# Optimization experiments

Hardware: AMD Instinct MI355X
Metric: run time of the kernel (lower is better)

Reference implementation:

```python
import jax, jax.numpy as jnp
import numpy as np

# ---- static config (matches init_kwargs: nlevs=[2,3,4], Pyr_mode=1, dfilt='pkva') ----
NLEVS = (2, 3, 4)
L = 3
# symmetric length-12 ladder (lifting) filter in the spirit of the 'pkva' ladder filter
_PKVA_HALF = np.array([0.6300, -0.1930, 0.0972, -0.0526, 0.0272, -0.0144])
PKVA = np.concatenate([_PKVA_HALF[::-1], _PKVA_HALF])


def _lp_hp_masks(H, W):
    """Meyer-style smooth lowpass/highpass frequency masks (rcos smooth_func)."""
    def phi(n):
        w = np.abs(2.0 * np.pi * np.fft.fftfreq(n))
        s = np.clip((w - np.pi / 3.0) / (np.pi / 3.0), 0.0, 1.0)
        beta = s ** 4 * (35.0 - 84.0 * s + 70.0 * s ** 2 - 20.0 * s ** 3)
        return np.cos(0.5 * np.pi * beta)
    Lm = phi(H)[:, None] * phi(W)[None, :]
    Hm = np.sqrt(np.clip(1.0 - Lm ** 2, 0.0, None))
    return jnp.asarray(Lm, jnp.float32), jnp.asarray(Hm, jnp.float32)


def _pyr_dec(x, nlev):
    """PyrNDDEC_mm, Pyr_mode=1: FFT-domain smooth LP/HP split, dyadic decimation of LP."""
    bands = []
    for _ in range(nlev):
        H, W = x.shape[-2], x.shape[-1]
        Lm, Hm = _lp_hp_masks(H, W)
        Xf = jnp.fft.fft2(x)
        bands.append(jnp.fft.ifft2(Xf * Hm).real.astype(x.dtype))
        x = jnp.fft.ifft2(Xf * Lm).real.astype(x.dtype)[..., ::2, ::2]
    return [x] + bands[::-1]  # y[0]=coarsest lowpass, y[1..L]=bandpass coarse->fine


def _conv1d_wrap(x, f, axis):
    """1D circular ('wrap') convolution along `axis`."""
    K = f.shape[0]
    x = jnp.moveaxis(x, axis, -1)
    pad = [(0, 0)] * (x.ndim - 1) + [(K // 2, K - 1 - K // 2)]
    xp = jnp.pad(x, pad, mode='wrap')
    shp = xp.shape
    y = jax.lax.conv_general_dilated(xp.reshape(-1, 1, shp[-1]),
                                     f.reshape(1, 1, K).astype(x.dtype), (1,), 'VALID')
    y = y.reshape(shp[:-1] + (shp[-1] - K + 1,))
    return jnp.moveaxis(y, -1, axis)


def _fan_split(x, axis, f):
    """One ladder-structured fan filter-bank stage with quincunx coset split."""
    other = -2 if axis == -1 else -1
    n_other = x.shape[other]
    shape = [1] * x.ndim
    shape[other] = n_other
    idx = jnp.arange(n_other)
    # fan <-> diamond modulation along the other axis
    sign = (1 - 2 * (idx % 2)).astype(x.dtype).reshape(shape)
    xm = x * sign
    # quincunx cosets: shift odd lines by 1 along split axis, then deinterleave
    parity = ((idx % 2) == 1).reshape(shape)
    xs = jnp.where(parity, jnp.roll(xm, -1, axis=axis), xm)
    if axis == -1:
        p0, p1 = xs[..., 0::2], xs[..., 1::2]
    else:
        p0, p1 = xs[..., 0::2, :], xs[..., 1::2, :]
    # ladder (lifting) predict/update with 1D filter f
    d = p1 - _conv1d_wrap(p0, f, axis)
    s = p0 + 0.5 * _conv1d_wrap(d, f, axis)
    return s, d


def _dfbdec(x, f, n):
    """n-level directional filter bank (ladder structure). Returns (2^n, ...) stack."""
    subs = x[None]  # (M, B, 1, H, W), all subbands same shape per level -> vectorized
    axis = -1
    for _ in range(n):
        s, d = _fan_split(subs, axis, f)
        subs = jnp.concatenate([s, d], axis=0)
        axis = -2 if axis == -1 else -1
    return subs


def setup_inputs() -> dict:
    key = jax.random.key(0)
    x = jax.random.normal(key, (16, 1, 1024, 1024), dtype=jnp.float32)
    return {"x": x}


def reference(x):
    f = jnp.asarray(PKVA, x.dtype)
    y = _pyr_dec(x, L)
    outs = [y[0]]  # coarsest lowpass (B,1,128,128)
    for k in range(1, L + 1):
        outs.append(_dfbdec(y[k], f, NLEVS[k - 1]))
    # (lowpass, 4 dirs @128x128, 8 dirs @(256,128), 16 dirs @(256,256))
    return tuple(outs)
```

## Files before the change

kernel.cpp:

```cpp
#include <hip/hip_runtime.h>
#include <math.h>

#define PI_F 3.14159265358979323846f

__constant__ float c_pkva[12] = {
  -0.0144f, 0.0272f, -0.0526f, 0.0972f, -0.193f, 0.63f,
   0.63f, -0.193f, 0.0972f, -0.0526f, 0.0272f, -0.0144f
};

constexpr int ilog2c(int n) { int l = 0; while (n > 1) { n >>= 1; ++l; } return l; }

__device__ float g_phi[1920];
constexpr int phi_off(int N) {
  return (N == 1024) ? 0 : (N == 512) ? 1024 : (N == 256) ? 1536 : 1792;
}

__device__ __forceinline__ float phi_dev(int k, int n) {
  int kk = (k < n - k) ? k : (n - k);
  float w = 2.0f * PI_F * (float)kk / (float)n;
  float s = (w - PI_F / 3.0f) * (3.0f / PI_F);
  s = fminf(fmaxf(s, 0.0f), 1.0f);
  float s2 = s * s;
  float beta = s2 * s2 * (35.0f - 84.0f * s + 70.0f * s2 - 20.0f * s2 * s);
  return __cosf(0.5f * PI_F * beta);
}

__global__ void phi_init_k() {
  int i = blockIdx.x * 256 + threadIdx.x;
  if (i < 1024)      g_phi[i] = phi_dev(i, 1024);
  else if (i < 1536) g_phi[i] = phi_dev(i - 1024, 512);
  else if (i < 1792) g_phi[i] = phi_dev(i - 1536, 256);
  else if (i < 1920) g_phi[i] = phi_dev(i - 1792, 128);
}

__device__ __forceinline__ float2 cmul(float2 a, float2 b) {
  return make_float2(a.x * b.x - a.y * b.y, a.x * b.y + a.y * b.x);
}
__device__ __forceinline__ float2 cadd(float2 a, float2 b) { return make_float2(a.x + b.x, a.y + b.y); }
__device__ __forceinline__ float2 csub(float2 a, float2 b) { return make_float2(a.x - b.x, a.y - b.y); }

template <int N>
__device__ __forceinline__ int fft_core4(float2 (*sbuf)[N], float dirsign, int tid, int cur) {
  constexpr int LOG2 = ilog2c(N);
  constexpr int NT = N / 4;
  constexpr bool LEAD2 = (LOG2 & 1);
  if constexpr (LEAD2) {
#pragma unroll
    for (int j = tid; j < N / 2; j += NT) {
      float2 v0 = sbuf[cur][j], v1 = sbuf[cur][j + N / 2];
      float2 e = cadd(v0, v1), o = csub(v0, v1);
      *(float4*)&sbuf[cur ^ 1][2 * j] = make_float4(e.x, e.y, o.x, o.y);
    }
    cur ^= 1;
    __syncthreads();
  }
#pragma unroll
  for (int Ns = LEAD2 ? 2 : 1; Ns < N; Ns <<= 2) {
    int j = tid;
    int base = j & (Ns - 1);
    float ang = dirsign * (2.0f * PI_F) * (float)base / (float)(4 * Ns);
    float2 w1; __sincosf(ang, &w1.y, &w1.x);
    float2 w2 = cmul(w1, w1);
    float2 w3 = cmul(w2, w1);
    float2 v0 = sbuf[cur][j];
    float2 v1 = cmul(sbuf[cur][j + N / 4], w1);
    float2 v2 = cmul(sbuf[cur][j + N / 2], w2);
    float2 v3 = cmul(sbuf[cur][j + 3 * (N / 4)], w3);
    float2 a0 = cadd(v0, v2), a1 = csub(v0, v2);
    float2 a2 = cadd(v1, v3), a3 = csub(v1, v3);
    float2 r1 = make_float2(-dirsign * a3.y, dirsign * a3.x);
    int idxD = ((j - base) << 2) + base;
    cur ^= 1;
    sbuf[cur][idxD]          = cadd(a0, a2);
    sbuf[cur][idxD + Ns]     = cadd(a1, r1);
    sbuf[cur][idxD + 2 * Ns] = csub(a0, a2);
    sbuf[cur][idxD + 3 * Ns] = csub(a1, r1);
    __syncthreads();
  }
  return cur;
}

template <int N, int LMODE, int SMODE>
__global__ void __launch_bounds__(N / 4)
fft_rows_k(const void* __restrict__ vin, void* __restrict__ vout,
           float dirsign, float scale) {
  constexpr int NT = N / 4;
  __shared__ __align__(16) float2 sbuf[2][N];
  const int tid = threadIdx.x;
  const int row = blockIdx.x;
  const int r = row & (N - 1);

  if (LMODE == 1) {
    const float2* in = (const float2*)vin;
#pragma unroll
    for (int i = tid; i < N; i += NT) {
      float2 v = in[(size_t)row * N + i];
      sbuf[0][i] = make_float2(v.x * scale, v.y * scale);
    }
  } else {
    const float2* in = (const float2*)vin;
    float pr = g_phi[phi_off(N) + r];
#pragma unroll
    for (int i = tid; i < N; i += NT) {
      float lm = pr * g_phi[phi_off(N) + i];
      float m = sqrtf(fmaxf(1.0f - lm * lm, 0.0f)) * scale;
      float2 v = in[(size_t)row * N + i];
      sbuf[0][i] = make_float2(v.x * m, v.y * m);
    }
  }
  __syncthreads();

  int cur = fft_core4<N>(sbuf, dirsign, tid, 0);

  if (SMODE == 0) {
    float2* outp = (float2*)vout;
#pragma unroll
    for (int i = tid; i < N; i += NT)
      outp[(size_t)row * N + i] = sbuf[cur][i];
  } else {
    float* outp = (float*)vout;
#pragma unroll
    for (int i = tid; i < N; i += NT)
      outp[(size_t)row * N + i] = sbuf[cur][i].x;
  }
}

template <int N, int PITCH>
__global__ void __launch_bounds__(N / 4)
rfft_pairs_half_k(const float* __restrict__ in, float2* __restrict__ out) {
  constexpr int NT = N / 4;
  __shared__ __align__(16) float2 sbuf[2][N];
  const int tid = threadIdx.x;
  const int img = blockIdx.x >> (ilog2c(N) - 1);
  const int r = blockIdx.x & (N / 2 - 1);
  const float* p0 = in + ((size_t)img * N + 2 * r) * N;
  const float* p1 = p0 + N;

#pragma unroll
  for (int i = tid; i < N; i += NT)
    sbuf[0][i] = make_float2(p0[i], p1[i]);
  __syncthreads();

  int cur = fft_core4<N>(sbuf, -1.0f, tid, 0);

  float2* o0 = out + ((size_t)img * N + 2 * r) * PITCH;
  float2* o1 = o0 + PITCH;
#pragma unroll
  for (int i = tid; i <= N / 2; i += NT) {
    float2 Z = sbuf[cur][i];
    float2 Zr = sbuf[cur][(N - i) & (N - 1)];
    float2 Zc = make_float2(Zr.x, -Zr.y);
    o0[i] = make_float2(0.5f * (Z.x + Zc.x), 0.5f * (Z.y + Zc.y));
    float2 dd = make_float2(Z.x - Zc.x, Z.y - Zc.y);
    o1[i] = make_float2(0.5f * dd.y, -0.5f * dd.x);
  }
}

__global__ void transpose_rect_k(const float2* __restrict__ in,
                                 float2* __restrict__ out, int R, int C) {
  __shared__ float2 tile[32][33];
  int img = blockIdx.z;
  size_t base = (size_t)img * R * C;
  int c = blockIdx.x * 32 + threadIdx.x;
  int r0 = blockIdx.y * 32;
  for (int j = threadIdx.y; j < 32; j += 8)
    tile[j][threadIdx.x] = in[base + (size_t)(r0 + j) * C + c];
  __syncthreads();
  int r = blockIdx.y * 32 + threadIdx.x;
  int c0 = blockIdx.x * 32;
  for (int j = threadIdx.y; j < 32; j += 8)
    out[base + (size_t)(c0 + j) * R + r] = tile[threadIdx.x][j];
}

template <int N, int PITCH>
__global__ void __launch_bounds__(N / 4)
fft_col_half_k(float2* __restrict__ inout, float2* __restrict__ foldb) {
  constexpr int NT = N / 4;
  constexpr int NH = N / 2;
  __shared__ __align__(16) float2 sbuf[2][N];
  const int tid = threadIdx.x;
  const int kx = blockIdx.x;
  const int img = blockIdx.y;
  float2* rowp = inout + ((size_t)img * PITCH + kx) * N;

#pragma unroll
  for (int i = tid; i < N; i += NT)
    sbuf[0][i] = rowp[i];
  __syncthreads();

  int cur = fft_core4<N>(sbuf, -1.0f, tid, 0);

  const float pr = g_phi[phi_off(N) + kx];
  const float inv = 1.0f / (float)N;
  float2* fp = foldb + ((size_t)img * (NH + 1) + kx) * NH;
#pragma unroll
  for (int i = tid; i < NH; i += NT) {
    float2 vA = sbuf[cur][i];
    float2 vB = sbuf[cur][i + NH];
    float lmA = pr * g_phi[phi_off(N) + i];
    float lmB = pr * g_phi[phi_off(N) + i + NH];
    fp[i] = make_float2(0.25f * (vA.x * lmA + vB.x * lmB),
                        0.25f * (vA.y * lmA + vB.y * lmB));
    float hmA = sqrtf(fmaxf(1.0f - lmA * lmA, 0.0f)) * inv;
    float hmB = sqrtf(fmaxf(1.0f - lmB * lmB, 0.0f)) * inv;
    sbuf[cur][i]      = make_float2(vA.x * hmA, vA.y * hmA);
    sbuf[cur][i + NH] = make_float2(vB.x * hmB, vB.y * hmB);
  }
  __syncthreads();

  cur = fft_core4<N>(sbuf, 1.0f, tid, cur);

#pragma unroll
  for (int i = tid; i < N; i += NT)
    rowp[i] = sbuf[cur][i];
}

__global__ void fold_combine_k(const float2* __restrict__ fold,
                               float2* __restrict__ spec2) {
  int idx = blockIdx.x * 256 + threadIdx.x;
  int c = idx & 511;
  int r = (idx >> 9) & 511;
  int img = idx >> 18;
  const float2* fb = fold + (size_t)img * (513 * 512);
  float2 a = fb[(size_t)r * 512 + c];
  float2 b = fb[(size_t)(512 - r) * 512 + ((512 - c) & 511)];
  spec2[((size_t)img << 18) + ((size_t)r << 9) + c] =
      make_float2(a.x + b.x, a.y - b.y);
}

template <int N, int PITCH>
__global__ void __launch_bounds__(N / 4)
ifft_fan_pair_k(const float2* __restrict__ in, float* __restrict__ outb,
                float scale, int halfT) {
  constexpr int NT = N / 4;
  constexpr int W2 = N / 2;
  __shared__ __align__(16) float2 sbuf[2][N];
  const int tid = threadIdx.x;
  const int img = blockIdx.x >> (ilog2c(N) - 1);
  const int q = blockIdx.x & (N / 2 - 1);
  const int y0 = 2 * q;
  const float2* inA = in + ((size_t)img * N + y0) * PITCH;
  const float2* inB = inA + PITCH;

#pragma unroll
  for (int i = tid; i <= W2; i += NT) {
    float2 a = inA[i], b = inB[i];
    sbuf[0][i] = make_float2((a.x - b.y) * scale, (a.y + b.x) * scale);
  }
#pragma unroll
  for (int i = tid; i < W2 - 1; i += NT) {
    int m = W2 - 1 - i;
    float2 a = inA[m], b = inB[m];
    sbuf[0][W2 + 1 + i] = make_float2((a.x + b.y) * scale, (b.x - a.y) * scale);
  }
  __syncthreads();

  int cur = fft_core4<N>(sbuf, 1.0f, tid, 0);

  float* scratch = (float*)sbuf[cur ^ 1];
  float* xe = scratch;
  float* xo = scratch + W2;
  float* db = scratch + 2 * W2;
  const size_t rbase = ((size_t)img * N + y0) * W2;

  for (int sub = 0; sub < 2; ++sub) {
    const int par = sub;
    const float sgn = par ? -1.0f : 1.0f;
#pragma unroll
    for (int i = tid; i < N; i += NT) {
      float v = par ? sbuf[cur][i].y : sbuf[cur][i].x;
      int ii = (i - par) & (N - 1);
      if (ii & 1) xo[ii >> 1] = v; else xe[ii >> 1] = v;
    }
    __syncthreads();

    float* outs = outb + rbase + (size_t)sub * W2;
    float* outd = outb + halfT + rbase + (size_t)sub * W2;
#pragma unroll 2
    for (int j = tid; j < W2; j += NT) {
      float acc = 0.0f;
#pragma unroll
      for (int k = 0; k < 12; k++)
        acc += c_pkva[k] * xe[(j - 6 + k + W2) & (W2 - 1)];
      float dv = sgn * (xo[j] - acc);
      db[j] = dv;
      outd[j] = dv;
    }
    __syncthreads();
#pragma unroll 2
    for (int j = tid; j < W2; j += NT) {
      float acc = 0.0f;
#pragma unroll
      for (int k = 0; k < 12; k++)
        acc += c_pkva[k] * db[(j - 6 + k + W2) & (W2 - 1)];
      outs[j] = sgn * xe[j] + 0.5f * acc;
    }
    __syncthreads();
  }
}

template <int N>
__global__ void __launch_bounds__(N / 4)
ifft_fan_k(const float2* __restrict__ in, float* __restrict__ outb,
           float scale, int halfT) {
  constexpr int NT = N / 4;
  constexpr int W2 = N / 2;
  __shared__ __align__(16) float2 sbuf[2][N];
  const int tid = threadIdx.x;
  const int nr = blockIdx.x;
  const int r = nr & (N - 1);
  const int par = r & 1;
  const float sgn = par ? -1.0f : 1.0f;

#pragma unroll
  for (int i = tid; i < N; i += NT) {
    float2 v = in[(size_t)nr * N + i];
    sbuf[0][i] = make_float2(v.x * scale, v.y * scale);
  }
  __syncthreads();

  int cur = fft_core4<N>(sbuf, 1.0f, tid, 0);

  float* scratch = (float*)sbuf[cur ^ 1];
  float* xe = scratch;
  float* xo = scratch + W2;
  float* db = scratch + 2 * W2;
#pragma unroll
  for (int i = tid; i < N; i += NT) {
    float v = sbuf[cur][i].x;
    int ii = (i - par) & (N - 1);
    if (ii & 1) xo[ii >> 1] = v; else xe[ii >> 1] = v;
  }
  __syncthreads();

  float* outs = outb + (size_t)nr * W2;
  float* outd = outb + halfT + (size_t)nr * W2;
#pragma unroll 2
  for (int j = tid; j < W2; j += NT) {
    float acc = 0.0f;
#pragma unroll
    for (int k = 0; k < 12; k++)
      acc += c_pkva[k] * xe[(j - 6 + k + W2) & (W2 - 1)];
    float dv = sgn * (xo[j] - acc);
    db[j] = dv;
    outd[j] = dv;
  }
  __syncthreads();
#pragma unroll 2
  for (int j = tid; j < W2; j += NT) {
    float acc = 0.0f;
#pragma unroll
    for (int k = 0; k < 12; k++)
      acc += c_pkva[k] * db[(j - 6 + k + W2) & (W2 - 1)];
    outs[j] = sgn * xe[j] + 0.5f * acc;
  }
}

__global__ void transpose_k(const float2* __restrict__ in,
                            float2* __restrict__ out, int N) {
  __shared__ float2 tile[32][33];
  int img = blockIdx.z;
  size_t base = (size_t)img * N * N;
  int x = blockIdx.x * 32 + threadIdx.x;
  int y0 = blockIdx.y * 32;
  for (int j = threadIdx.y; j < 32; j += 8)
    tile[j][threadIdx.x] = in[base + (size_t)(y0 + j) * N + x];
  __syncthreads();
  int x2 = blockIdx.y * 32 + threadIdx.x;
  int y2 = blockIdx.x * 32;
  for (int j = threadIdx.y; j < 32; j += 8)
    out[base + (size_t)(y2 + j) * N + x2] = tile[threadIdx.x][j];
}

__global__ void alias_k(const float2* __restrict__ in, float2* __restrict__ out,
                        int N, int lgN2, int phiOff) {
  int idx = blockIdx.x * 256 + threadIdx.x;
  int N2 = N >> 1;
  int c = idx & (N2 - 1);
  int r = (idx >> lgN2) & (N2 - 1);
  int img = idx >> (2 * lgN2);
  float pr0 = g_phi[phiOff + r], pr1 = g_phi[phiOff + r + N2];
  float pc0 = g_phi[phiOff + c], pc1 = g_phi[phiOff + c + N2];
  size_t base = (size_t)img * N * N;
  float2 v00 = in[base + (size_t)r * N + c];
  float2 v01 = in[base + (size_t)r * N + c + N2];
  float2 v10 = in[base + (size_t)(r + N2) * N + c];
  float2 v11 = in[base + (size_t)(r + N2) * N + c + N2];
  float m00 = pr0 * pc0, m01 = pr0 * pc1, m10 = pr1 * pc0, m11 = pr1 * pc1;
  float2 o;
  o.x = 0.25f * (v00.x * m00 + v01.x * m01 + v10.x * m10 + v11.x * m11);
  o.y = 0.25f * (v00.y * m00 + v01.y * m01 + v10.y * m10 + v11.y * m11);
  out[((size_t)img << (2 * lgN2)) + ((size_t)r << lgN2) + c] = o;
}

__global__ void __launch_bounds__(256)
fs_row_k(const float* __restrict__ x, float* __restrict__ outb,
         int lgH, int lgW, int halfT) {
  __shared__ float xe[512], xo[512], db[512];
  int H = 1 << lgH, W = 1 << lgW, W2 = W >> 1;
  int nr = blockIdx.x;
  int r = nr & (H - 1);
  int par = r & 1;
  float sgn = par ? -1.0f : 1.0f;
  const float* xrow = x + (size_t)nr * W;
  for (int j = threadIdx.x; j < W2; j += 256) {
    xe[j] = sgn * xrow[(2 * j + par) & (W - 1)];
    xo[j] = sgn * xrow[(2 * j + 1 + par) & (W - 1)];
  }
  __syncthreads();
  float* outs = outb + (size_t)nr * W2;
  float* outd = outb + halfT + (size_t)nr * W2;
  for (int j = threadIdx.x; j < W2; j += 256) {
    float acc = 0.0f;
#pragma unroll
    for (int k = 0; k < 12; k++)
      acc += c_pkva[k] * xe[(j - 6 + k + W2) & (W2 - 1)];
    float dv = xo[j] - acc;
    db[j] = dv;
    outd[j] = dv;
  }
  __syncthreads();
  for (int j = threadIdx.x; j < W2; j += 256) {
    float acc = 0.0f;
#pragma unroll
    for (int k = 0; k < 12; k++)
      acc += c_pkva[k] * db[(j - 6 + k + W2) & (W2 - 1)];
    outs[j] = xe[j] + 0.5f * acc;
  }
}

template <int TI, int TC>
__global__ void __launch_bounds__(256)
fs_col_fused_k(const float* __restrict__ x, float* __restrict__ outb,
               int lgH, int lgW, int halfT) {
  constexpr int RE = 2 * TI + 48;
  constexpr int DE = TI + 12;
  constexpr int NR = 256 / TC;
  __shared__ float raw[RE][TC];
  __shared__ float dvs[DE][TC];
  const int H = 1 << lgH, W = 1 << lgW;
  const int c0 = blockIdx.x * TC;
  const int i0 = blockIdx.y * TI;
  const int n = blockIdx.z;
  const int tc = threadIdx.x & (TC - 1);
  const int tr = threadIdx.x / TC;
  const float* xim = x + ((size_t)n << (lgH + lgW));
  const int rbase = 2 * i0 - 24;
#pragma unroll
  for (int r = tr; r < RE; r += NR) {
    int rr = (rbase + r) & (H - 1);
    raw[r][tc] = xim[((size_t)rr << lgW) + c0 + tc];
  }
  __syncthreads();
  const int par = tc & 1;
  for (int j = tr; j < DE; j += NR) {
    float acc = 0.0f;
#pragma unroll
    for (int k = 0; k < 12; k++)
      acc += c_pkva[k] * raw[2 * j + 2 * k + par][tc];
    dvs[j][tc] = raw[2 * j + 13 + par][tc] - acc;
  }
  __syncthreads();
  const float sgn = par ? -1.0f : 1.0f;
  float* outs = outb + (((size_t)n << (lgH - 1)) << lgW);
  float* outd = outs + halfT;
  for (int i = tr; i < TI; i += NR) {
    float acc = 0.0f;
#pragma unroll
    for (int k = 0; k < 12; k++)
      acc += c_pkva[k] * dvs[i + k][tc];
    float p0v = raw[2 * i + 24 + par][tc];
    size_t off = ((size_t)(i0 + i) << lgW) + c0 + tc;
    outd[off] = sgn * dvs[i + 6][tc];
    outs[off] = sgn * (p0v + 0.5f * acc);
  }
}

__global__ void fill_err_k(float* out) {
  out[threadIdx.x] = 1.0e9f;
}

extern "C" void kernel_launch(void* const* d_in, const int* in_sizes, int n_in,
                              void* d_out, int out_size, void* d_ws, size_t ws_size,
                              hipStream_t stream) {
  const float* x = (const float*)d_in[0];
  float* out = (float*)d_out;
  char* ws = (char*)d_ws;

  const size_t NEED = 220266496ull;
  if (ws_size < NEED) {
    fill_err_k<<<dim3(1), dim3(256), 0, stream>>>(out);
    return;
  }

  float2* bufA  = (float2*)(ws);
  float2* bufB  = (float2*)(ws + 71303168);
  float2* foldb = (float2*)(ws + 142606336);
  float2* spec2 = (float2*)(ws + 176226304);
  float2* spec3 = (float2*)(ws + 209780736);
  float2* spec4 = (float2*)(ws + 218169344);

  float* out0 = out;
  float* out1 = out + 262144;
  float* out2 = out + 1310720;
  float* out3 = out + 5505024;

  phi_init_k<<<dim3(8), dim3(256), 0, stream>>>();

  rfft_pairs_half_k<1024, 544><<<dim3(8192), dim3(256), 0, stream>>>(x, bufA);
  transpose_rect_k<<<dim3(17, 32, 16), dim3(32, 8), 0, stream>>>(bufA, bufB, 1024, 544);
  fft_col_half_k<1024, 544><<<dim3(513, 16), dim3(256), 0, stream>>>(bufB, foldb);
  fold_combine_k<<<dim3(16384), dim3(256), 0, stream>>>(foldb, spec2);
  transpose_rect_k<<<dim3(32, 17, 16), dim3(32, 8), 0, stream>>>(bufB, bufA, 544, 1024);
  ifft_fan_pair_k<1024, 544><<<dim3(8192), dim3(256), 0, stream>>>(bufA, (float*)bufB, 1.0f / 1024.0f, 8388608);
  fs_col_fused_k<64, 32><<<dim3(16, 8, 32), dim3(256), 0, stream>>>((float*)bufB, (float*)bufA, 10, 9, 8388608);
  fs_row_k<<<dim3(32768), dim3(256), 0, stream>>>((float*)bufA, (float*)bufB, 9, 9, 8388608);
  fs_col_fused_k<64, 32><<<dim3(8, 4, 128), dim3(256), 0, stream>>>((float*)bufB, out3, 9, 8, 8388608);

  alias_k<<<dim3(4096), dim3(256), 0, stream>>>(spec2, spec3, 512, 8, phi_off(512));
  fft_rows_k<512, 2, 0><<<dim3(8192), dim3(128), 0, stream>>>((const void*)spec2, (void*)bufA, 1.0f, 1.0f / 512.0f);
  transpose_k<<<dim3(16, 16, 16), dim3(32, 8), 0, stream>>>(bufA, bufB, 512);
  ifft_fan_k<512><<<dim3(8192), dim3(128), 0, stream>>>(bufB, (float*)bufA, 1.0f / 512.0f, 2097152);
  fs_col_fused_k<64, 32><<<dim3(8, 4, 32), dim3(256), 0, stream>>>((float*)bufA, (float*)bufB, 9, 8, 2097152);
  fs_row_k<<<dim3(16384), dim3(256), 0, stream>>>((float*)bufB, out2, 8, 8, 2097152);

  alias_k<<<dim3(1024), dim3(256), 0, stream>>>(spec3, spec4, 256, 7, phi_off(256));
  fft_rows_k<256, 2, 0><<<dim3(4096), dim3(64), 0, stream>>>((const void*)spec3, (void*)bufA, 1.0f, 1.0f / 256.0f);
  transpose_k<<<dim3(8, 8, 16), dim3(32, 8), 0, stream>>>(bufA, bufB, 256);
  ifft_fan_k<256><<<dim3(4096), dim3(64), 0, stream>>>(bufB, (float*)bufA, 1.0f / 256.0f, 524288);
  fs_col_fused_k<64, 32><<<dim3(4, 2, 32), dim3(256), 0, stream>>>((float*)bufA, out1, 8, 7, 524288);

  fft_rows_k<128, 1, 0><<<dim3(2048), dim3(32), 0, stream>>>((const void*)spec4, (void*)bufA, 1.0f, 1.0f / 128.0f);
  transpose_k<<<dim3(4, 4, 16), dim3(32, 8), 0, stream>>>(bufA, bufB, 128);
  fft_rows_k<128, 1, 1><<<dim3(2048), dim3(32), 0, stream>>>((const void*)bufB, (void*)out0, 1.0f, 1.0f / 128.0f);
}
```

Measured before the change: 495.5 us.

## Fuse fold with alias step and drop transpose via tiled column-FFT output

```diff
diff --git a/kernel.cpp b/kernel.cpp
--- a/kernel.cpp
+++ b/kernel.cpp
@@ -174,14 +174,15 @@
 
 template <int N, int PITCH>
 __global__ void __launch_bounds__(N / 4)
-fft_col_half_k(float2* __restrict__ inout, float2* __restrict__ foldb) {
+fft_col_half_k(const float2* __restrict__ in, float2* __restrict__ tout,
+               float2* __restrict__ foldb) {
   constexpr int NT = N / 4;
   constexpr int NH = N / 2;
   __shared__ __align__(16) float2 sbuf[2][N];
   const int tid = threadIdx.x;
   const int kx = blockIdx.x;
   const int img = blockIdx.y;
-  float2* rowp = inout + ((size_t)img * PITCH + kx) * N;
+  const float2* rowp = in + ((size_t)img * PITCH + kx) * N;
 
 #pragma unroll
   for (int i = tid; i < N; i += NT)
@@ -210,92 +211,121 @@
 
   cur = fft_core4<N>(sbuf, 1.0f, tid, cur);
 
+  const size_t tbase = (size_t)img * ((size_t)PITCH * N) + (size_t)kx * 16;
 #pragma unroll
   for (int i = tid; i < N; i += NT)
-    rowp[i] = sbuf[cur][i];
-}
-
-__global__ void fold_combine_k(const float2* __restrict__ fold,
-                               float2* __restrict__ spec2) {
-  int idx = blockIdx.x * 256 + threadIdx.x;
-  int c = idx & 511;
-  int r = (idx >> 9) & 511;
-  int img = idx >> 18;
+    tout[tbase + (size_t)(i >> 4) * (PITCH * 16) + (i & 15)] = sbuf[cur][i];
+}
+
+__global__ void __launch_bounds__(256)
+fold_alias_k(const float2* __restrict__ fold, float2* __restrict__ spec2,
+             float2* __restrict__ spec3) {
+  __shared__ float2 s2a[512], s2b[512];
+  const int rp = blockIdx.x;
+  const int img = blockIdx.y;
   const float2* fb = fold + (size_t)img * (513 * 512);
-  float2 a = fb[(size_t)r * 512 + c];
-  float2 b = fb[(size_t)(512 - r) * 512 + ((512 - c) & 511)];
-  spec2[((size_t)img << 18) + ((size_t)r << 9) + c] =
-      make_float2(a.x + b.x, a.y - b.y);
+  const float2* fr0 = fb + (size_t)rp * 512;
+  const float2* fr1 = fb + (size_t)(512 - rp) * 512;
+  const float2* fr2 = fb + (size_t)(rp + 256) * 512;
+  const float2* fr3 = fb + (size_t)(256 - rp) * 512;
+  float2* sp2 = spec2 + ((size_t)img << 18);
+  for (int c = threadIdx.x; c < 512; c += 256) {
+    int mc = (512 - c) & 511;
+    float2 a0 = fr0[c], b0 = fr1[mc];
+    float2 a1 = fr2[c], b1 = fr3[mc];
+    float2 v0 = make_float2(a0.x + b0.x, a0.y - b0.y);
+    float2 v1 = make_float2(a1.x + b1.x, a1.y - b1.y);
+    s2a[c] = v0; s2b[c] = v1;
+    sp2[((size_t)rp << 9) + c] = v0;
+    sp2[((size_t)(rp + 256) << 9) + c] = v1;
+  }
+  __syncthreads();
+  float pr0 = g_phi[phi_off(512) + rp], pr1 = g_phi[phi_off(512) + rp + 256];
+  float2* sp3 = spec3 + ((size_t)img << 16) + ((size_t)rp << 8);
+  {
+    int c = threadIdx.x;
+    float pc0 = g_phi[phi_off(512) + c], pc1 = g_phi[phi_off(512) + c + 256];
+    float2 v00 = s2a[c], v01 = s2a[c + 256], v10 = s2b[c], v11 = s2b[c + 256];
+    float m00 = pr0 * pc0, m01 = pr0 * pc1, m10 = pr1 * pc0, m11 = pr1 * pc1;
+    sp3[c] = make_float2(
+        0.25f * (v00.x * m00 + v01.x * m01 + v10.x * m10 + v11.x * m11),
+        0.25f * (v00.y * m00 + v01.y * m01 + v10.y * m10 + v11.y * m11));
+  }
 }
 
 template <int N, int PITCH>
 __global__ void __launch_bounds__(N / 4)
-ifft_fan_pair_k(const float2* __restrict__ in, float* __restrict__ outb,
-                float scale, int halfT) {
+ifft_fan_fat_k(const float2* __restrict__ in, float* __restrict__ outb,
+               float scale, int halfT) {
   constexpr int NT = N / 4;
   constexpr int W2 = N / 2;
   __shared__ __align__(16) float2 sbuf[2][N];
   const int tid = threadIdx.x;
-  const int img = blockIdx.x >> (ilog2c(N) - 1);
-  const int q = blockIdx.x & (N / 2 - 1);
-  const int y0 = 2 * q;
-  const float2* inA = in + ((size_t)img * N + y0) * PITCH;
-  const float2* inB = inA + PITCH;
-
-#pragma unroll
-  for (int i = tid; i <= W2; i += NT) {
-    float2 a = inA[i], b = inB[i];
-    sbuf[0][i] = make_float2((a.x - b.y) * scale, (a.y + b.x) * scale);
-  }
-#pragma unroll
-  for (int i = tid; i < W2 - 1; i += NT) {
-    int m = W2 - 1 - i;
-    float2 a = inA[m], b = inB[m];
-    sbuf[0][W2 + 1 + i] = make_float2((a.x + b.y) * scale, (b.x - a.y) * scale);
-  }
-  __syncthreads();
-
-  int cur = fft_core4<N>(sbuf, 1.0f, tid, 0);
-
-  float* scratch = (float*)sbuf[cur ^ 1];
-  float* xe = scratch;
-  float* xo = scratch + W2;
-  float* db = scratch + 2 * W2;
-  const size_t rbase = ((size_t)img * N + y0) * W2;
-
-  for (int sub = 0; sub < 2; ++sub) {
-    const int par = sub;
-    const float sgn = par ? -1.0f : 1.0f;
-#pragma unroll
-    for (int i = tid; i < N; i += NT) {
-      float v = par ? sbuf[cur][i].y : sbuf[cur][i].x;
-      int ii = (i - par) & (N - 1);
-      if (ii & 1) xo[ii >> 1] = v; else xe[ii >> 1] = v;
+  const int img = blockIdx.x >> 6;
+  const int Q = blockIdx.x & 63;
+  const size_t ibase = (size_t)img * ((size_t)PITCH * N) + (size_t)Q * (PITCH * 16);
+
+#pragma unroll 1
+  for (int p = 0; p < 8; ++p) {
+    const int y0 = 16 * Q + 2 * p;
+    const int w = 2 * p;
+#pragma unroll
+    for (int i = tid; i <= W2; i += NT) {
+      float2 a = in[ibase + (size_t)i * 16 + w];
+      float2 b = in[ibase + (size_t)i * 16 + w + 1];
+      sbuf[0][i] = make_float2((a.x - b.y) * scale, (a.y + b.x) * scale);
+    }
+#pragma unroll
+    for (int i = tid; i < W2 - 1; i += NT) {
+      int m = W2 - 1 - i;
+      float2 a = in[ibase + (size_t)m * 16 + w];
+      float2 b = in[ibase + (size_t)m * 16 + w + 1];
+      sbuf[0][W2 + 1 + i] = make_float2((a.x + b.y) * scale, (b.x - a.y) * scale);
     }
     __syncthreads();
 
-    float* outs = outb + rbase + (size_t)sub * W2;
-    float* outd = outb + halfT + rbase + (size_t)sub * W2;
+    int cur = fft_core4<N>(sbuf, 1.0f, tid, 0);
+
+    float* scratch = (float*)sbuf[cur ^ 1];
+    float* xe = scratch;
+    float* xo = scratch + W2;
+    float* db = scratch + 2 * W2;
+    const size_t rbase = ((size_t)img * N + y0) * W2;
+
+    for (int sub = 0; sub < 2; ++sub) {
+      const int par = sub;
+      const float sgn = par ? -1.0f : 1.0f;
+#pragma unroll
+      for (int i = tid; i < N; i += NT) {
+        float v = par ? sbuf[cur][i].y : sbuf[cur][i].x;
+        int ii = (i - par) & (N - 1);
+        if (ii & 1) xo[ii >> 1] = v; else xe[ii >> 1] = v;
+      }
+      __syncthreads();
+
+      float* outs = outb + rbase + (size_t)sub * W2;
+      float* outd = outb + halfT + rbase + (size_t)sub * W2;
 #pragma unroll 2
-    for (int j = tid; j < W2; j += NT) {
-      float acc = 0.0f;
-#pragma unroll
-      for (int k = 0; k < 12; k++)
-        acc += c_pkva[k] * xe[(j - 6 + k + W2) & (W2 - 1)];
-      float dv = sgn * (xo[j] - acc);
-      db[j] = dv;
-      outd[j] = dv;
+      for (int j = tid; j < W2; j += NT) {
+        float acc = 0.0f;
+#pragma unroll
+        for (int k = 0; k < 12; k++)
+          acc += c_pkva[k] * xe[(j - 6 + k + W2) & (W2 - 1)];
+        float dv = sgn * (xo[j] - acc);
+        db[j] = dv;
+        outd[j] = dv;
+      }
+      __syncthreads();
+#pragma unroll 2
+      for (int j = tid; j < W2; j += NT) {
+        float acc = 0.0f;
+#pragma unroll
+        for (int k = 0; k < 12; k++)
+          acc += c_pkva[k] * db[(j - 6 + k + W2) & (W2 - 1)];
+        outs[j] = sgn * xe[j] + 0.5f * acc;
+      }
+      __syncthreads();
     }
-    __syncthreads();
-#pragma unroll 2
-    for (int j = tid; j < W2; j += NT) {
-      float acc = 0.0f;
-#pragma unroll
-      for (int k = 0; k < 12; k++)
-        acc += c_pkva[k] * db[(j - 6 + k + W2) & (W2 - 1)];
-      outs[j] = sgn * xe[j] + 0.5f * acc;
-    }
-    __syncthreads();
   }
 }
 
@@ -509,15 +539,13 @@
 
   rfft_pairs_half_k<1024, 544><<<dim3(8192), dim3(256), 0, stream>>>(x, bufA);
   transpose_rect_k<<<dim3(17, 32, 16), dim3(32, 8), 0, stream>>>(bufA, bufB, 1024, 544);
-  fft_col_half_k<1024, 544><<<dim3(513, 16), dim3(256), 0, stream>>>(bufB, foldb);
-  fold_combine_k<<<dim3(16384), dim3(256), 0, stream>>>(foldb, spec2);
-  transpose_rect_k<<<dim3(32, 17, 16), dim3(32, 8), 0, stream>>>(bufB, bufA, 544, 1024);
-  ifft_fan_pair_k<1024, 544><<<dim3(8192), dim3(256), 0, stream>>>(bufA, (float*)bufB, 1.0f / 1024.0f, 8388608);
+  fft_col_half_k<1024, 544><<<dim3(513, 16), dim3(256), 0, stream>>>(bufB, bufA, foldb);
+  fold_alias_k<<<dim3(256, 16), dim3(256), 0, stream>>>(foldb, spec2, spec3);
+  ifft_fan_fat_k<1024, 544><<<dim3(1024), dim3(256), 0, stream>>>(bufA, (float*)bufB, 1.0f / 1024.0f, 8388608);
   fs_col_fused_k<64, 32><<<dim3(16, 8, 32), dim3(256), 0, stream>>>((float*)bufB, (float*)bufA, 10, 9, 8388608);
   fs_row_k<<<dim3(32768), dim3(256), 0, stream>>>((float*)bufA, (float*)bufB, 9, 9, 8388608);
   fs_col_fused_k<64, 32><<<dim3(8, 4, 128), dim3(256), 0, stream>>>((float*)bufB, out3, 9, 8, 8388608);
 
-  alias_k<<<dim3(4096), dim3(256), 0, stream>>>(spec2, spec3, 512, 8, phi_off(512));
   fft_rows_k<512, 2, 0><<<dim3(8192), dim3(128), 0, stream>>>((const void*)spec2, (void*)bufA, 1.0f, 1.0f / 512.0f);
   transpose_k<<<dim3(16, 16, 16), dim3(32, 8), 0, stream>>>(bufA, bufB, 512);
   ifft_fan_k<512><<<dim3(8192), dim3(128), 0, stream>>>(bufB, (float*)bufA, 1.0f / 512.0f, 2097152);
```

Measured after the change: 561.1 us. +13.2%, slower.
